# Kernel optimization log

Measured on AMD Instinct MI355X. Metric: run time of the kernel, lower is better.

## Reference

```python
import jax, jax.numpy as jnp
import numpy as np

N_NODES = 100000
N_EDGES = 1000000

def _gcn_conv(x, W, b, src, dst, n_nodes):
    # PyG GCNConv: linear first, then symmetric-normalized aggregation with self loops
    x = x @ W  # [N, F_out]
    loop = jnp.arange(n_nodes, dtype=src.dtype)
    src2 = jnp.concatenate([src, loop])
    dst2 = jnp.concatenate([dst, loop])
    deg = jax.ops.segment_sum(jnp.ones(src2.shape[0], x.dtype), dst2, num_segments=n_nodes)
    dinv = jnp.where(deg > 0, jax.lax.rsqrt(deg), 0.0)
    norm = dinv[src2] * dinv[dst2]  # [E+N]
    msgs = x[src2] * norm[:, None]  # gather + scale
    out = jax.ops.segment_sum(msgs, dst2, num_segments=n_nodes)  # scatter-add
    return out + b

def _pair_norm_si(x):
    # mode 'PN-SI', scale=1
    x = x - x.mean(axis=0)
    row_norm = jnp.sqrt(1e-6 + jnp.sum(x * x, axis=1, keepdims=True))
    return x / row_norm

def setup_inputs() -> dict:
    key = jax.random.key(0)
    k1, k2, k3, k4 = jax.random.split(key, 4)
    in_c, hid_c, out_c = 256, 64, 40
    x = jax.random.normal(k1, (N_NODES, in_c), dtype=jnp.float32)
    edge_index = jax.random.randint(k2, (2, N_EDGES), 0, N_NODES, dtype=jnp.int64)
    W1 = jax.random.normal(k3, (in_c, hid_c), dtype=jnp.float32) / np.sqrt(in_c)
    b1 = jnp.zeros((hid_c,), jnp.float32)
    W2 = jax.random.normal(k4, (hid_c, out_c), dtype=jnp.float32) / np.sqrt(hid_c)
    b2 = jnp.zeros((out_c,), jnp.float32)
    return {"x": x, "edge_index": edge_index, "W1": W1, "b1": b1, "W2": W2, "b2": b2}

def reference(x, edge_index, W1, b1, W2, b2):
    src, dst = edge_index[0], edge_index[1]
    n = x.shape[0]
    h = jax.nn.relu(_gcn_conv(x, W1, b1, src, dst, n))
    h = _gcn_conv(h, W2, b2, src, dst, n)
    h = _pair_norm_si(h)
    return jax.nn.log_softmax(h, axis=1)
```

## Files before the change

### kernel.cpp

```cpp
#include <hip/hip_runtime.h>
#include <hip/hip_fp16.h>
#include <math.h>

#define F_IN  256
#define F_HID 64
#define F_OUT 40
#define HS2_LD 64

typedef _Float16 h8 __attribute__((ext_vector_type(8)));
typedef _Float16 h4 __attribute__((ext_vector_type(4)));
typedef float f4 __attribute__((ext_vector_type(4)));

__global__ void k_degw(const int* __restrict__ dst, unsigned* __restrict__ degc, int E,
                       const float* __restrict__ W1, const float* __restrict__ W2,
                       __half* __restrict__ Wt, __half* __restrict__ W2t) {
    int i = blockIdx.x * 256 + threadIdx.x;
    if (i < E) {
        atomicAdd(&degc[dst[i]], 1u);
        return;
    }
    int j = i - E;
    if (j < 16384) {
        int k = j >> 6, n = j & 63;
        Wt[n * 256 + k] = __float2half(W1[j]);
    } else if (j < 20480) {
        int jj = j - 16384;
        int n = jj >> 6, k = jj & 63;
        W2t[n * 64 + k] = __float2half((n < F_OUT) ? W2[k * F_OUT + n] : 0.f);
    }
}

__global__ __launch_bounds__(256) void k_scan(const unsigned* __restrict__ degc,
                                              unsigned* __restrict__ aggf,
                                              unsigned* __restrict__ ticket,
                                              unsigned* __restrict__ rowptr,
                                              float* __restrict__ dinv,
                                              unsigned* __restrict__ cursor,
                                              float* __restrict__ colsum, int N) {
    __shared__ unsigned s[256];
    __shared__ unsigned sTick, sPfx, sTot;
    int tid = threadIdx.x;
    if (tid == 0) sTick = atomicAdd(ticket, 1u);
    if (blockIdx.x == 0 && tid < 64) colsum[tid] = 0.f;
    __syncthreads();
    unsigned b = sTick;
    int i = (int)b * 256 + tid;
    unsigned d = (i < N) ? degc[i] : 0u;
    unsigned v = (i < N) ? ((d + 8u) & ~7u) : 0u;
    s[tid] = v;
    __syncthreads();
    for (int off = 1; off < 256; off <<= 1) {
        unsigned t = (tid >= off) ? s[tid - off] : 0u;
        __syncthreads();
        s[tid] += t;
        __syncthreads();
    }
    unsigned incl = s[tid];
    if (tid == 255) {
        sTot = s[255];
        atomicExch(&aggf[b], s[255] | 0x40000000u);
    }
    __syncthreads();
    if (tid < 64) {
        int lane = tid;
        unsigned run = 0;
        int base = (int)b - 1;
        while (base >= 0) {
            int idx = base - lane;
            unsigned t = 0;
            if (idx >= 0) {
                do { t = atomicAdd(&aggf[idx], 0u); } while ((t >> 30) == 0u);
            }
            unsigned long long pmask = __ballot(idx >= 0 && (t >> 30) == 3u);
            if (pmask) {
                int L = __ffsll((unsigned long long)pmask) - 1;
                unsigned contrib = (lane <= L) ? (t & 0x3FFFFFFFu) : 0u;
                #pragma unroll
                for (int off = 32; off >= 1; off >>= 1) contrib += __shfl_xor(contrib, off, 64);
                run += contrib;
                break;
            } else {
                unsigned contrib = (idx >= 0) ? (t & 0x3FFFFFFFu) : 0u;
                #pragma unroll
                for (int off = 32; off >= 1; off >>= 1) contrib += __shfl_xor(contrib, off, 64);
                run += contrib;
                base -= 64;
            }
        }
        if (lane == 0) {
            sPfx = run;
            atomicExch(&aggf[b], (run + sTot) | 0xC0000000u);
        }
    }
    __syncthreads();
    unsigned pfx = sPfx;
    if (i < N) {
        rowptr[i] = pfx + incl - v;
        dinv[i] = rsqrtf((float)d + 1.0f);
        cursor[i] = 0u;
        if (i == N - 1) rowptr[N] = pfx + incl;
    }
    if (i == 0) dinv[N] = 1.0f;
}

__global__ __launch_bounds__(256) void k_fillpad(const int* __restrict__ src, const int* __restrict__ dst,
                          const unsigned* __restrict__ degc,
                          const unsigned* __restrict__ rowptr, unsigned* __restrict__ cursor,
                          unsigned* __restrict__ colp, int E, int N) {
    int r  = blockIdx.x & 7;
    int sb = blockIdx.x >> 3;
    int S  = gridDim.x >> 3;
    int lo = (int)(((long long)N * r) >> 3);
    int hi = (int)(((long long)N * (r + 1)) >> 3);
    int tid = threadIdx.x;
    int stride = S * 256;
    for (int t = sb * 256 + tid; t < E; t += stride) {
        int d = dst[t];
        if (d >= lo && d < hi) {
            unsigned p = atomicAdd(&cursor[d], 1u);
            colp[rowptr[d] + p] = (unsigned)src[t];
        }
    }
    int npad = (hi - lo) * 8;
    for (int z = sb * 256 + tid; z < npad; z += stride) {
        int i = lo + (z >> 3), j = z & 7;
        unsigned d = degc[i];
        unsigned slot = d + (unsigned)j;
        if (slot < ((d + 8u) & ~7u))
            colp[rowptr[i] + slot] = (j == 0) ? (unsigned)i : (unsigned)N;
    }
}

__global__ __launch_bounds__(256) void k_mm1(const float* __restrict__ x,
                                             const __half* __restrict__ Wth,
                                             const float* __restrict__ dinv,
                                             __half* __restrict__ hs1o, int N) {
    const _Float16* Wt = (const _Float16*)Wth;
    _Float16* hs1 = (_Float16*)hs1o;
    int tid = threadIdx.x;
    int lane = tid & 63;
    int wv = tid >> 6;
    int m15 = lane & 15;
    int q = lane >> 4;
    int node0 = blockIdx.x * 64 + wv * 16;
    int arow = node0 + m15;
    bool ok = (arow < N);
    const float* xr = x + (size_t)arow * F_IN + q * 8;

    f4 acc[4];
    #pragma unroll
    for (int nt = 0; nt < 4; ++nt) acc[nt] = (f4){0.f, 0.f, 0.f, 0.f};

    #pragma unroll
    for (int kt = 0; kt < 8; ++kt) {
        float4 v0, v1;
        if (ok) {
            v0 = *(const float4*)(xr + kt * 32);
            v1 = *(const float4*)(xr + kt * 32 + 4);
        } else {
            v0 = make_float4(0.f, 0.f, 0.f, 0.f);
            v1 = v0;
        }
        h8 a = { (_Float16)v0.x, (_Float16)v0.y, (_Float16)v0.z, (_Float16)v0.w,
                 (_Float16)v1.x, (_Float16)v1.y, (_Float16)v1.z, (_Float16)v1.w };
        #pragma unroll
        for (int nt = 0; nt < 4; ++nt) {
            h8 b = *(const h8*)(Wt + (nt * 16 + m15) * 256 + kt * 32 + q * 8);
            acc[nt] = __builtin_amdgcn_mfma_f32_16x16x32_f16(a, b, acc[nt], 0, 0, 0);
        }
    }

    #pragma unroll
    for (int nt = 0; nt < 4; ++nt) {
        #pragma unroll
        for (int rr = 0; rr < 4; ++rr) {
            int node = node0 + q * 4 + rr;
            if (node <= N) {
                float din = (node < N) ? dinv[node] : 1.0f;
                hs1[(size_t)node * F_HID + nt * 16 + m15] = (_Float16)(acc[nt][rr] * din);
            }
        }
    }
}

__global__ __launch_bounds__(256) void k_agg1(const unsigned* __restrict__ rowptr,
                                              const unsigned* __restrict__ colp,
                                              const float* __restrict__ dinv,
                                              const __half* __restrict__ hs1o,
                                              const float* __restrict__ bias1,
                                              __half* __restrict__ agg1o, int N) {
    const _Float16* hp = (const _Float16*)hs1o;
    _Float16* agg1h = (_Float16*)agg1o;
    int lane = threadIdx.x & 63;
    int w = blockIdx.x * 4 + (threadIdx.x >> 6);
    int n0 = 4 * w;
    if (n0 >= N) return;
    int g = lane >> 3, c = lane & 7;

    float acc[4][8];
    #pragma unroll
    for (int s = 0; s < 4; ++s)
        #pragma unroll
        for (int j = 0; j < 8; ++j) acc[s][j] = 0.f;

    unsigned e[4], en[4], idx[4];
    #pragma unroll
    for (int s = 0; s < 4; ++s) {
        int nd = n0 + s;
        if (nd < N) { e[s] = rowptr[nd]; en[s] = rowptr[nd + 1]; }
        else        { e[s] = 0; en[s] = 0; }
    }
    #pragma unroll
    for (int s = 0; s < 4; ++s) {
        unsigned ec = (e[s] < en[s]) ? e[s] : (en[s] - 8u);
        ec = (ec > e[s]) ? e[s] : ec;
        idx[s] = colp[ec + g];
    }

    while (e[0] < en[0] || e[1] < en[1] || e[2] < en[2] || e[3] < en[3]) {
        float msk[4];
        h8 v[4];
        #pragma unroll
        for (int s = 0; s < 4; ++s) msk[s] = (e[s] < en[s]) ? 1.f : 0.f;
        #pragma unroll
        for (int s = 0; s < 4; ++s) v[s] = *(const h8*)(hp + (size_t)idx[s] * F_HID + c * 8);
        #pragma unroll
        for (int s = 0; s < 4; ++s) {
            e[s] += 8;
            unsigned ec = (e[s] < en[s]) ? e[s] : (en[s] - 8u);
            ec = (ec > e[s]) ? e[s] : ec;
            idx[s] = colp[ec + g];
        }
        #pragma unroll
        for (int s = 0; s < 4; ++s)
            #pragma unroll
            for (int j = 0; j < 8; ++j) acc[s][j] += (float)v[s][j] * msk[s];
    }

    #pragma unroll
    for (int off = 8; off <= 32; off <<= 1)
        #pragma unroll
        for (int s = 0; s < 4; ++s)
            #pragma unroll
            for (int j = 0; j < 8; ++j) acc[s][j] += __shfl_xor(acc[s][j], off, 64);

    if (g == 0) {
        float bv[8];
        *(float4*)&bv[0] = *(const float4*)(bias1 + c * 8);
        *(float4*)&bv[4] = *(const float4*)(bias1 + c * 8 + 4);
        #pragma unroll
        for (int s = 0; s < 4; ++s) {
            int nd = n0 + s;
            if (nd < N) {
                float din = dinv[nd];
                h8 ho;
                #pragma unroll
                for (int j = 0; j < 8; ++j) ho[j] = (_Float16)fmaxf(acc[s][j] * din + bv[j], 0.f);
                *(h8*)(agg1h + (size_t)nd * F_HID + c * 8) = ho;
            }
        }
    }
}

#define AS 72
__global__ __launch_bounds__(256) void k_mm2(const __half* __restrict__ agg1o,
                                             const __half* __restrict__ W2th,
                                             const float* __restrict__ dinv,
                                             __half* __restrict__ hs2o, int N) {
    __shared__ _Float16 sA[64 * AS];
    const _Float16* agg1h = (const _Float16*)agg1o;
    const _Float16* W2t = (const _Float16*)W2th;
    _Float16* hs2 = (_Float16*)hs2o;
    int tid = threadIdx.x;
    int lane = tid & 63;
    int wv = tid >> 6;
    int m15 = lane & 15;
    int q = lane >> 4;
    int nbase = blockIdx.x * 64;

    h8 bf[2];
    #pragma unroll
    for (int kt = 0; kt < 2; ++kt)
        bf[kt] = *(const h8*)(W2t + (wv * 16 + m15) * 64 + kt * 32 + q * 8);

    #pragma unroll
    for (int p = 0; p < 2; ++p) {
        int idx = p * 256 + tid;
        int row = idx >> 3;
        int c8  = idx & 7;
        int node = nbase + row;
        h8 v;
        if (node < N) v = *(const h8*)(agg1h + (size_t)node * F_HID + c8 * 8);
        else          v = (h8){0, 0, 0, 0, 0, 0, 0, 0};
        *(h8*)&sA[row * AS + c8 * 8] = v;
    }
    __syncthreads();

    f4 acc[4];
    #pragma unroll
    for (int mt = 0; mt < 4; ++mt) acc[mt] = (f4){0.f, 0.f, 0.f, 0.f};
    #pragma unroll
    for (int kt = 0; kt < 2; ++kt) {
        #pragma unroll
        for (int mt = 0; mt < 4; ++mt) {
            h8 a = *(const h8*)&sA[(mt * 16 + m15) * AS + kt * 32 + q * 8];
            acc[mt] = __builtin_amdgcn_mfma_f32_16x16x32_f16(a, bf[kt], acc[mt], 0, 0, 0);
        }
    }

    #pragma unroll
    for (int mt = 0; mt < 4; ++mt) {
        #pragma unroll
        for (int r = 0; r < 4; ++r) {
            int node = nbase + mt * 16 + q * 4 + r;
            if (node <= N) {
                float din = (node < N) ? dinv[node] : 1.0f;
                hs2[(size_t)node * HS2_LD + wv * 16 + m15] = (_Float16)(acc[mt][r] * din);
            }
        }
    }
}

__global__ __launch_bounds__(256) void k_agg2(const unsigned* __restrict__ rowptr,
                                              const unsigned* __restrict__ colp,
                                              const float* __restrict__ dinv,
                                              const __half* __restrict__ hs2o,
                                              float* __restrict__ out,
                                              float* __restrict__ colsum, int N) {
    __shared__ float part[4][8][8];
    const _Float16* hp = (const _Float16*)hs2o;
    int lane = threadIdx.x & 63;
    int wv = threadIdx.x >> 6;
    int g = lane >> 3, c = lane & 7;
    int nwaves = gridDim.x * 4;
    float csum[8];
    #pragma unroll
    for (int j = 0; j < 8; ++j) csum[j] = 0.f;

    for (int w = blockIdx.x * 4 + wv; 4 * w < N; w += nwaves) {
        int n0 = 4 * w;
        float acc[4][8];
        #pragma unroll
        for (int s = 0; s < 4; ++s)
            #pragma unroll
            for (int j = 0; j < 8; ++j) acc[s][j] = 0.f;

        unsigned e[4], en[4], idx[4];
        #pragma unroll
        for (int s = 0; s < 4; ++s) {
            int nd = n0 + s;
            if (nd < N) { e[s] = rowptr[nd]; en[s] = rowptr[nd + 1]; }
            else        { e[s] = 0; en[s] = 0; }
        }
        #pragma unroll
        for (int s = 0; s < 4; ++s) {
            unsigned ec = (e[s] < en[s]) ? e[s] : (en[s] - 8u);
            ec = (ec > e[s]) ? e[s] : ec;
            idx[s] = colp[ec + g];
        }

        while (e[0] < en[0] || e[1] < en[1] || e[2] < en[2] || e[3] < en[3]) {
            float msk[4];
            h8 v[4];
            #pragma unroll
            for (int s = 0; s < 4; ++s) msk[s] = (e[s] < en[s]) ? 1.f : 0.f;
            #pragma unroll
            for (int s = 0; s < 4; ++s) v[s] = *(const h8*)(hp + (size_t)idx[s] * HS2_LD + c * 8);
            #pragma unroll
            for (int s = 0; s < 4; ++s) {
                e[s] += 8;
                unsigned ec = (e[s] < en[s]) ? e[s] : (en[s] - 8u);
                ec = (ec > e[s]) ? e[s] : ec;
                idx[s] = colp[ec + g];
            }
            #pragma unroll
            for (int s = 0; s < 4; ++s)
                #pragma unroll
                for (int j = 0; j < 8; ++j) acc[s][j] += (float)v[s][j] * msk[s];
        }

        #pragma unroll
        for (int off = 8; off <= 32; off <<= 1)
            #pragma unroll
            for (int s = 0; s < 4; ++s)
                #pragma unroll
                for (int j = 0; j < 8; ++j) acc[s][j] += __shfl_xor(acc[s][j], off, 64);

        if (g == 0) {
            #pragma unroll
            for (int s = 0; s < 4; ++s) {
                int nd = n0 + s;
                if (nd < N) {
                    float din = dinv[nd];
                    #pragma unroll
                    for (int j = 0; j < 8; ++j) { acc[s][j] *= din; csum[j] += acc[s][j]; }
                    if (c < 5) {
                        *(float4*)(out + (size_t)nd * F_OUT + c * 8) =
                            make_float4(acc[s][0], acc[s][1], acc[s][2], acc[s][3]);
                        *(float4*)(out + (size_t)nd * F_OUT + c * 8 + 4) =
                            make_float4(acc[s][4], acc[s][5], acc[s][6], acc[s][7]);
                    }
                }
            }
        }
    }

    if (g == 0) {
        #pragma unroll
        for (int j = 0; j < 8; ++j) part[wv][c][j] = csum[j];
    }
    __syncthreads();
    int tid = threadIdx.x;
    if (tid < F_OUT) {
        int cc = tid >> 3, jj = tid & 7;
        float s = part[0][cc][jj] + part[1][cc][jj] + part[2][cc][jj] + part[3][cc][jj];
        atomicAdd(&colsum[tid], s);
    }
}

__global__ __launch_bounds__(128) void k_final(float* __restrict__ out,
                                               const float* __restrict__ colsum, int N) {
    __shared__ float sMean[F_OUT];
    if (threadIdx.x < F_OUT) sMean[threadIdx.x] = colsum[threadIdx.x] * (1.0f / (float)N);
    __syncthreads();
    int n = blockIdx.x * blockDim.x + threadIdx.x;
    if (n >= N) return;
    float* row = out + (size_t)n * F_OUT;
    float v[F_OUT];
    float ss = 0.f;
    #pragma unroll
    for (int f = 0; f < F_OUT; ++f) {
        float t = row[f] - sMean[f];
        v[f] = t;
        ss += t * t;
    }
    float scale = 1.0f / sqrtf(ss + 1e-6f);
    float m = -1e30f;
    #pragma unroll
    for (int f = 0; f < F_OUT; ++f) {
        float y = v[f] * scale;
        v[f] = y;
        m = fmaxf(m, y);
    }
    float sum = 0.f;
    #pragma unroll
    for (int f = 0; f < F_OUT; ++f) sum += expf(v[f] - m);
    float lse = logf(sum);
    #pragma unroll
    for (int f = 0; f < F_OUT; ++f) row[f] = v[f] - m - lse;
}

extern "C" void kernel_launch(void* const* d_in, const int* in_sizes, int n_in,
                              void* d_out, int out_size, void* d_ws, size_t ws_size,
                              hipStream_t stream) {
    const float* x  = (const float*)d_in[0];
    const int*   ei = (const int*)d_in[1];
    const float* W1 = (const float*)d_in[2];
    const float* b1 = (const float*)d_in[3];
    const float* W2 = (const float*)d_in[4];
    float* out = (float*)d_out;

    int N = in_sizes[0] / F_IN;
    int E = in_sizes[1] / 2;
    const int* src = ei;
    const int* dst = ei + E;

    char* p = (char*)d_ws;
    auto alloc = [&](size_t bytes) { char* r = p; p += (bytes + 127) & ~(size_t)127; return r; };
    unsigned* degc   = (unsigned*)alloc((size_t)N * 4);
    unsigned* aggf   = (unsigned*)alloc(512 * 4);
    unsigned* ticket = (unsigned*)alloc(4);
    char* zend = p;
    unsigned* cursor = (unsigned*)alloc((size_t)N * 4);
    float*    colsum = (float*)   alloc(64 * 4);
    unsigned* rowptr = (unsigned*)alloc((size_t)(N + 1) * 4);
    unsigned* colp   = (unsigned*)alloc((size_t)(E + 8 * N + 8) * 4);
    float*    dinv   = (float*)   alloc((size_t)(N + 1) * 4);
    __half*   agg1h  = (__half*)  alloc((size_t)64 * (N + 1) * 2);
    __half*   hs1    = (__half*)  alloc((size_t)64 * (N + 1) * 2);
    __half*   hs2    = (__half*)  alloc((size_t)64 * (N + 1) * 2);
    __half*   Wt     = (__half*)  alloc((size_t)16384 * 2);
    __half*   W2t    = (__half*)  alloc((size_t)4096 * 2);

    hipMemsetAsync(d_ws, 0, (size_t)(zend - (char*)d_ws), stream);

    int nA = (N + 255) / 256;
    k_degw<<<(E + 20480 + 255) / 256, 256, 0, stream>>>(dst, degc, E, W1, W2, Wt, W2t);
    k_scan<<<nA, 256, 0, stream>>>(degc, aggf, ticket, rowptr, dinv, cursor, colsum, N);
    k_fillpad<<<2048, 256, 0, stream>>>(src, dst, degc, rowptr, cursor, colp, E, N);
    k_mm1<<<(N + 63) / 64, 256, 0, stream>>>(x, Wt, dinv, hs1, N);
    int nodes4 = (N + 3) / 4;
    k_agg1<<<(nodes4 + 3) / 4, 256, 0, stream>>>(rowptr, colp, dinv, hs1, b1, agg1h, N);
    k_mm2<<<(N + 64) / 64, 256, 0, stream>>>(agg1h, W2t, dinv, hs2, N);
    k_agg2<<<2048, 256, 0, stream>>>(rowptr, colp, dinv, hs2, out, colsum, N);
    k_final<<<(N + 127) / 128, 128, 0, stream>>>(out, colsum, N);
}
```

Baseline: 392.6 us.

## Fuse CSR fill with first matmul and first aggregation with second matmul

```diff
diff --git a/kernel.cpp b/kernel.cpp
--- a/kernel.cpp
+++ b/kernel.cpp
@@ -8,7 +8,6 @@
 #define HS2_LD 64
 
 typedef _Float16 h8 __attribute__((ext_vector_type(8)));
-typedef _Float16 h4 __attribute__((ext_vector_type(4)));
 typedef float f4 __attribute__((ext_vector_type(4)));
 
 __global__ void k_degw(const int* __restrict__ dst, unsigned* __restrict__ degc, int E,
@@ -16,7 +15,8 @@
                        __half* __restrict__ Wt, __half* __restrict__ W2t) {
     int i = blockIdx.x * 256 + threadIdx.x;
     if (i < E) {
-        atomicAdd(&degc[dst[i]], 1u);
+        int d = __builtin_nontemporal_load(dst + i);
+        atomicAdd(&degc[d], 1u);
         return;
     }
     int j = i - E;
@@ -103,49 +103,50 @@
     if (i == 0) dinv[N] = 1.0f;
 }
 
-__global__ __launch_bounds__(256) void k_fillpad(const int* __restrict__ src, const int* __restrict__ dst,
+#define FILLB 1024
+__global__ __launch_bounds__(256) void k_fillmm1(const int* __restrict__ src, const int* __restrict__ dst,
                           const unsigned* __restrict__ degc,
                           const unsigned* __restrict__ rowptr, unsigned* __restrict__ cursor,
-                          unsigned* __restrict__ colp, int E, int N) {
-    int r  = blockIdx.x & 7;
-    int sb = blockIdx.x >> 3;
-    int S  = gridDim.x >> 3;
-    int lo = (int)(((long long)N * r) >> 3);
-    int hi = (int)(((long long)N * (r + 1)) >> 3);
+                          unsigned* __restrict__ colp,
+                          const float* __restrict__ x, const __half* __restrict__ Wth,
+                          const float* __restrict__ dinv, __half* __restrict__ hs1o,
+                          int E, int N) {
     int tid = threadIdx.x;
-    int stride = S * 256;
-    for (int t = sb * 256 + tid; t < E; t += stride) {
-        int d = dst[t];
-        if (d >= lo && d < hi) {
-            unsigned p = atomicAdd(&cursor[d], 1u);
-            colp[rowptr[d] + p] = (unsigned)src[t];
-        }
-    }
-    int npad = (hi - lo) * 8;
-    for (int z = sb * 256 + tid; z < npad; z += stride) {
-        int i = lo + (z >> 3), j = z & 7;
-        unsigned d = degc[i];
-        unsigned slot = d + (unsigned)j;
-        if (slot < ((d + 8u) & ~7u))
-            colp[rowptr[i] + slot] = (j == 0) ? (unsigned)i : (unsigned)N;
-    }
-}
-
-__global__ __launch_bounds__(256) void k_mm1(const float* __restrict__ x,
-                                             const __half* __restrict__ Wth,
-                                             const float* __restrict__ dinv,
-                                             __half* __restrict__ hs1o, int N) {
+    if ((int)blockIdx.x < FILLB) {
+        int r  = blockIdx.x & 3;
+        int sb = blockIdx.x >> 2;
+        int S  = FILLB >> 2;
+        int lo = (int)(((long long)N * r) >> 2);
+        int hi = (int)(((long long)N * (r + 1)) >> 2);
+        int stride = S * 256;
+        for (int t = sb * 256 + tid; t < E; t += stride) {
+            int d = __builtin_nontemporal_load(dst + t);
+            if (d >= lo && d < hi) {
+                int sv = __builtin_nontemporal_load(src + t);
+                unsigned p = atomicAdd(&cursor[d], 1u);
+                colp[rowptr[d] + p] = (unsigned)sv;
+            }
+        }
+        int npad = (hi - lo) * 8;
+        for (int z = sb * 256 + tid; z < npad; z += stride) {
+            int i = lo + (z >> 3), j = z & 7;
+            unsigned d = degc[i];
+            unsigned slot = d + (unsigned)j;
+            if (slot < ((d + 8u) & ~7u))
+                colp[rowptr[i] + slot] = (j == 0) ? (unsigned)i : (unsigned)N;
+        }
+        return;
+    }
     const _Float16* Wt = (const _Float16*)Wth;
     _Float16* hs1 = (_Float16*)hs1o;
-    int tid = threadIdx.x;
     int lane = tid & 63;
     int wv = tid >> 6;
     int m15 = lane & 15;
     int q = lane >> 4;
-    int node0 = blockIdx.x * 64 + wv * 16;
+    int node0 = ((int)blockIdx.x - FILLB) * 64 + wv * 16;
     int arow = node0 + m15;
     bool ok = (arow < N);
-    const float* xr = x + (size_t)arow * F_IN + q * 8;
+    const f4* xr = (const f4*)(x + (size_t)arow * F_IN + q * 8);
 
     f4 acc[4];
     #pragma unroll
@@ -153,16 +154,16 @@
 
     #pragma unroll
     for (int kt = 0; kt < 8; ++kt) {
-        float4 v0, v1;
+        f4 v0, v1;
         if (ok) {
-            v0 = *(const float4*)(xr + kt * 32);
-            v1 = *(const float4*)(xr + kt * 32 + 4);
+            v0 = __builtin_nontemporal_load(xr + kt * 8);
+            v1 = __builtin_nontemporal_load(xr + kt * 8 + 1);
         } else {
-            v0 = make_float4(0.f, 0.f, 0.f, 0.f);
+            v0 = (f4){0.f, 0.f, 0.f, 0.f};
             v1 = v0;
         }
-        h8 a = { (_Float16)v0.x, (_Float16)v0.y, (_Float16)v0.z, (_Float16)v0.w,
-                 (_Float16)v1.x, (_Float16)v1.y, (_Float16)v1.z, (_Float16)v1.w };
+        h8 a = { (_Float16)v0[0], (_Float16)v0[1], (_Float16)v0[2], (_Float16)v0[3],
+                 (_Float16)v1[0], (_Float16)v1[1], (_Float16)v1[2], (_Float16)v1[3] };
         #pragma unroll
         for (int nt = 0; nt < 4; ++nt) {
             h8 b = *(const h8*)(Wt + (nt * 16 + m15) * 256 + kt * 32 + q * 8);
@@ -183,128 +184,113 @@
     }
 }
 
-__global__ __launch_bounds__(256) void k_agg1(const unsigned* __restrict__ rowptr,
-                                              const unsigned* __restrict__ colp,
-                                              const float* __restrict__ dinv,
-                                              const __half* __restrict__ hs1o,
-                                              const float* __restrict__ bias1,
-                                              __half* __restrict__ agg1o, int N) {
+#define AS 72
+__global__ __launch_bounds__(256) void k_agg1mm2(const unsigned* __restrict__ rowptr,
+                                                 const unsigned* __restrict__ colp,
+                                                 const float* __restrict__ dinv,
+                                                 const __half* __restrict__ hs1o,
+                                                 const float* __restrict__ bias1,
+                                                 const __half* __restrict__ W2th,
+                                                 __half* __restrict__ hs2o, int N) {
+    __shared__ _Float16 sA[64 * AS];
     const _Float16* hp = (const _Float16*)hs1o;
-    _Float16* agg1h = (_Float16*)agg1o;
-    int lane = threadIdx.x & 63;
-    int w = blockIdx.x * 4 + (threadIdx.x >> 6);
-    int n0 = 4 * w;
-    if (n0 >= N) return;
-    int g = lane >> 3, c = lane & 7;
-
-    float acc[4][8];
-    #pragma unroll
-    for (int s = 0; s < 4; ++s)
-        #pragma unroll
-        for (int j = 0; j < 8; ++j) acc[s][j] = 0.f;
-
-    unsigned e[4], en[4], idx[4];
-    #pragma unroll
-    for (int s = 0; s < 4; ++s) {
-        int nd = n0 + s;
-        if (nd < N) { e[s] = rowptr[nd]; en[s] = rowptr[nd + 1]; }
-        else        { e[s] = 0; en[s] = 0; }
-    }
-    #pragma unroll
-    for (int s = 0; s < 4; ++s) {
-        unsigned ec = (e[s] < en[s]) ? e[s] : (en[s] - 8u);
-        ec = (ec > e[s]) ? e[s] : ec;
-        idx[s] = colp[ec + g];
-    }
-
-    while (e[0] < en[0] || e[1] < en[1] || e[2] < en[2] || e[3] < en[3]) {
-        float msk[4];
-        h8 v[4];
-        #pragma unroll
-        for (int s = 0; s < 4; ++s) msk[s] = (e[s] < en[s]) ? 1.f : 0.f;
-        #pragma unroll
-        for (int s = 0; s < 4; ++s) v[s] = *(const h8*)(hp + (size_t)idx[s] * F_HID + c * 8);
-        #pragma unroll
-        for (int s = 0; s < 4; ++s) {
-            e[s] += 8;
-            unsigned ec = (e[s] < en[s]) ? e[s] : (en[s] - 8u);
-            ec = (ec > e[s]) ? e[s] : ec;
-            idx[s] = colp[ec + g];
-        }
-        #pragma unroll
-        for (int s = 0; s < 4; ++s)
-            #pragma unroll
-            for (int j = 0; j < 8; ++j) acc[s][j] += (float)v[s][j] * msk[s];
-    }
-
-    #pragma unroll
-    for (int off = 8; off <= 32; off <<= 1)
-        #pragma unroll
-        for (int s = 0; s < 4; ++s)
-            #pragma unroll
-            for (int j = 0; j < 8; ++j) acc[s][j] += __shfl_xor(acc[s][j], off, 64);
-
-    if (g == 0) {
-        float bv[8];
-        *(float4*)&bv[0] = *(const float4*)(bias1 + c * 8);
-        *(float4*)&bv[4] = *(const float4*)(bias1 + c * 8 + 4);
-        #pragma unroll
-        for (int s = 0; s < 4; ++s) {
-            int nd = n0 + s;
-            if (nd < N) {
-                float din = dinv[nd];
-                h8 ho;
-                #pragma unroll
-                for (int j = 0; j < 8; ++j) ho[j] = (_Float16)fmaxf(acc[s][j] * din + bv[j], 0.f);
-                *(h8*)(agg1h + (size_t)nd * F_HID + c * 8) = ho;
-            }
-        }
-    }
-}
-
-#define AS 72
-__global__ __launch_bounds__(256) void k_mm2(const __half* __restrict__ agg1o,
-                                             const __half* __restrict__ W2th,
-                                             const float* __restrict__ dinv,
-                                             __half* __restrict__ hs2o, int N) {
-    __shared__ _Float16 sA[64 * AS];
-    const _Float16* agg1h = (const _Float16*)agg1o;
     const _Float16* W2t = (const _Float16*)W2th;
     _Float16* hs2 = (_Float16*)hs2o;
     int tid = threadIdx.x;
     int lane = tid & 63;
     int wv = tid >> 6;
+    int g = lane >> 3, c = lane & 7;
+    int nbase = blockIdx.x * 64;
+
+    float bv[8];
+    *(float4*)&bv[0] = *(const float4*)(bias1 + c * 8);
+    *(float4*)&bv[4] = *(const float4*)(bias1 + c * 8 + 4);
+
+    for (int it = 0; it < 4; ++it) {
+        int n0 = nbase + wv * 16 + it * 4;
+
+        float acc[4][8];
+        #pragma unroll
+        for (int s = 0; s < 4; ++s)
+            #pragma unroll
+            for (int j = 0; j < 8; ++j) acc[s][j] = 0.f;
+
+        unsigned e[4], en[4], idx[4];
+        #pragma unroll
+        for (int s = 0; s < 4; ++s) {
+            int nd = n0 + s;
+            if (nd < N) { e[s] = rowptr[nd]; en[s] = rowptr[nd + 1]; }
+            else        { e[s] = 0; en[s] = 0; }
+        }
+        #pragma unroll
+        for (int s = 0; s < 4; ++s) {
+            unsigned ec = (e[s] < en[s]) ? e[s] : (en[s] - 8u);
+            ec = (ec > e[s]) ? e[s] : ec;
+            idx[s] = colp[ec + g];
+        }
+
+        while (e[0] < en[0] || e[1] < en[1] || e[2] < en[2] || e[3] < en[3]) {
+            float msk[4];
+            h8 v[4];
+            #pragma unroll
+            for (int s = 0; s < 4; ++s) msk[s] = (e[s] < en[s]) ? 1.f : 0.f;
+            #pragma unroll
+            for (int s = 0; s < 4; ++s) v[s] = *(const h8*)(hp + (size_t)idx[s] * F_HID + c * 8);
+            #pragma unroll
+            for (int s = 0; s < 4; ++s) {
+                e[s] += 8;
+                unsigned ec = (e[s] < en[s]) ? e[s] : (en[s] - 8u);
+                ec = (ec > e[s]) ? e[s] : ec;
+                idx[s] = colp[ec + g];
+            }
+            #pragma unroll
+            for (int s = 0; s < 4; ++s)
+                #pragma unroll
+                for (int j = 0; j < 8; ++j) acc[s][j] += (float)v[s][j] * msk[s];
+        }
+
+        #pragma unroll
+        for (int off = 8; off <= 32; off <<= 1)
+            #pragma unroll
+            for (int s = 0; s < 4; ++s)
+                #pragma unroll
+                for (int j = 0; j < 8; ++j) acc[s][j] += __shfl_xor(acc[s][j], off, 64);
+
+        if (g == 0) {
+            #pragma unroll
+            for (int s = 0; s < 4; ++s) {
+                int nd = n0 + s;
+                int row = wv * 16 + it * 4 + s;
+                h8 ho;
+                if (nd < N) {
+                    float din = dinv[nd];
+                    #pragma unroll
+                    for (int j = 0; j < 8; ++j) ho[j] = (_Float16)fmaxf(acc[s][j] * din + bv[j], 0.f);
+                } else {
+                    ho = (h8){0, 0, 0, 0, 0, 0, 0, 0};
+                }
+                *(h8*)&sA[row * AS + c * 8] = ho;
+            }
+        }
+    }
+    __syncthreads();
+
     int m15 = lane & 15;
     int q = lane >> 4;
-    int nbase = blockIdx.x * 64;
-
     h8 bf[2];
     #pragma unroll
     for (int kt = 0; kt < 2; ++kt)
         bf[kt] = *(const h8*)(W2t + (wv * 16 + m15) * 64 + kt * 32 + q * 8);
 
-    #pragma unroll
-    for (int p = 0; p < 2; ++p) {
-        int idx = p * 256 + tid;
-        int row = idx >> 3;
-        int c8  = idx & 7;
-        int node = nbase + row;
-        h8 v;
-        if (node < N) v = *(const h8*)(agg1h + (size_t)node * F_HID + c8 * 8);
-        else          v = (h8){0, 0, 0, 0, 0, 0, 0, 0};
-        *(h8*)&sA[row * AS + c8 * 8] = v;
-    }
-    __syncthreads();
-
-    f4 acc[4];
-    #pragma unroll
-    for (int mt = 0; mt < 4; ++mt) acc[mt] = (f4){0.f, 0.f, 0.f, 0.f};
+    f4 acc2[4];
+    #pragma unroll
+    for (int mt = 0; mt < 4; ++mt) acc2[mt] = (f4){0.f, 0.f, 0.f, 0.f};
     #pragma unroll
     for (int kt = 0; kt < 2; ++kt) {
         #pragma unroll
         for (int mt = 0; mt < 4; ++mt) {
             h8 a = *(const h8*)&sA[(mt * 16 + m15) * AS + kt * 32 + q * 8];
-            acc[mt] = __builtin_amdgcn_mfma_f32_16x16x32_f16(a, bf[kt], acc[mt], 0, 0, 0);
+            acc2[mt] = __builtin_amdgcn_mfma_f32_16x16x32_f16(a, bf[kt], acc2[mt], 0, 0, 0);
         }
     }
 
@@ -315,7 +301,7 @@
             int node = nbase + mt * 16 + q * 4 + r;
             if (node <= N) {
                 float din = (node < N) ? dinv[node] : 1.0f;
-                hs2[(size_t)node * HS2_LD + wv * 16 + m15] = (_Float16)(acc[mt][r] * din);
+                hs2[(size_t)node * HS2_LD + wv * 16 + m15] = (_Float16)(acc2[mt][r] * din);
             }
         }
     }
@@ -426,28 +412,34 @@
     int n = blockIdx.x * blockDim.x + threadIdx.x;
     if (n >= N) return;
     float* row = out + (size_t)n * F_OUT;
-    float v[F_OUT];
+    float4 vr[10];
     float ss = 0.f;
     #pragma unroll
-    for (int f = 0; f < F_OUT; ++f) {
-        float t = row[f] - sMean[f];
-        v[f] = t;
-        ss += t * t;
+    for (int b = 0; b < 10; ++b) {
+        float4 t = *(const float4*)(row + b * 4);
+        t.x -= sMean[b * 4 + 0]; t.y -= sMean[b * 4 + 1];
+        t.z -= sMean[b * 4 + 2]; t.w -= sMean[b * 4 + 3];
+        vr[b] = t;
+        ss += t.x * t.x + t.y * t.y + t.z * t.z + t.w * t.w;
     }
     float scale = 1.0f / sqrtf(ss + 1e-6f);
     float m = -1e30f;
     #pragma unroll
-    for (int f = 0; f < F_OUT; ++f) {
-        float y = v[f] * scale;
-        v[f] = y;
-        m = fmaxf(m, y);
+    for (int b = 0; b < 10; ++b) {
+        vr[b].x *= scale; vr[b].y *= scale; vr[b].z *= scale; vr[b].w *= scale;
+        m = fmaxf(m, fmaxf(fmaxf(vr[b].x, vr[b].y), fmaxf(vr[b].z, vr[b].w)));
     }
     float sum = 0.f;
     #pragma unroll
-    for (int f = 0; f < F_OUT; ++f) sum += expf(v[f] - m);
-    float lse = logf(sum);
-    #pragma unroll
-    for (int f = 0; f < F_OUT; ++f) row[f] = v[f] - m - lse;
+    for (int b = 0; b < 10; ++b)
+        sum += expf(vr[b].x - m) + expf(vr[b].y - m) + expf(vr[b].z - m) + expf(vr[b].w - m);
+    float mlse = m + logf(sum);
+    #pragma unroll
+    for (int b = 0; b < 10; ++b) {
+        float4 t = vr[b];
+        t.x -= mlse; t.y -= mlse; t.z -= mlse; t.w -= mlse;
+        *(float4*)(row + b * 4) = t;
+    }
 }
 
 extern "C" void kernel_launch(void* const* d_in, const int* in_sizes, int n_in,
@@ -476,7 +468,6 @@
     unsigned* rowptr = (unsigned*)alloc((size_t)(N + 1) * 4);
     unsigned* colp   = (unsigned*)alloc((size_t)(E + 8 * N + 8) * 4);
     float*    dinv   = (float*)   alloc((size_t)(N + 1) * 4);
-    __half*   agg1h  = (__half*)  alloc((size_t)64 * (N + 1) * 2);
     __half*   hs1    = (__half*)  alloc((size_t)64 * (N + 1) * 2);
     __half*   hs2    = (__half*)  alloc((size_t)64 * (N + 1) * 2);
     __half*   Wt     = (__half*)  alloc((size_t)16384 * 2);
@@ -487,11 +478,10 @@
     int nA = (N + 255) / 256;
     k_degw<<<(E + 20480 + 255) / 256, 256, 0, stream>>>(dst, degc, E, W1, W2, Wt, W2t);
     k_scan<<<nA, 256, 0, stream>>>(degc, aggf, ticket, rowptr, dinv, cursor, colsum, N);
-    k_fillpad<<<2048, 256, 0, stream>>>(src, dst, degc, rowptr, cursor, colp, E, N);
-    k_mm1<<<(N + 63) / 64, 256, 0, stream>>>(x, Wt, dinv, hs1, N);
-    int nodes4 = (N + 3) / 4;
-    k_agg1<<<(nodes4 + 3) / 4, 256, 0, stream>>>(rowptr, colp, dinv, hs1, b1, agg1h, N);
-    k_mm2<<<(N + 64) / 64, 256, 0, stream>>>(agg1h, W2t, dinv, hs2, N);
+    int MB = (N + 63) / 64;
+    k_fillmm1<<<FILLB + MB, 256, 0, stream>>>(src, dst, degc, rowptr, cursor, colp,
+                                              x, Wt, dinv, hs1, E, N);
+    k_agg1mm2<<<(N + 64) / 64, 256, 0, stream>>>(rowptr, colp, dinv, hs1, b1, W2t, hs2, N);
     k_agg2<<<2048, 256, 0, stream>>>(rowptr, colp, dinv, hs2, out, colsum, N);
     k_final<<<(N + 127) / 128, 128, 0, stream>>>(out, colsum, N);
 }
```

Measured after the change: 400.0 us. About the same (+1.9%).
